# Performance work log

Measured on AMD Instinct MI355X. Metric: run time of the kernel, lower is better.

Reference implementation:

```python
import jax, jax.numpy as jnp
import numpy as np

GROUP_SIZE = 128
LORA_SCALING = 32.0 / 16.0  # lora_alpha / r


def _unpack_rows(q):
    # q: int32 [n, m] -> uint4 values [n*8, m], 8 nibbles per int32 along axis 0
    shifts = (jnp.arange(8, dtype=jnp.int32) * 4)
    vals = (q[:, None, :] >> shifts[None, :, None]) & 0xF
    return vals.reshape(q.shape[0] * 8, q.shape[1])


def _unpack_cols(q):
    # q: int32 [g, m] -> uint4 values [g, m*8], 8 nibbles per int32 along axis 1
    shifts = (jnp.arange(8, dtype=jnp.int32) * 4)
    vals = (q[:, :, None] >> shifts[None, None, :]) & 0xF
    return vals.reshape(q.shape[0], q.shape[1] * 8)


def setup_inputs() -> dict:
    key = jax.random.key(0)
    ks = jax.random.split(key, 6)
    in_f, out_f, tokens, r = 4096, 11008, 64, 16
    g = in_f // GROUP_SIZE  # 32 groups
    x = jax.random.normal(ks[0], (tokens, in_f), dtype=jnp.float32)
    qweight = jax.random.randint(ks[1], (in_f // 8, out_f), jnp.iinfo(jnp.int32).min, jnp.iinfo(jnp.int32).max, dtype=jnp.int32)
    qzeros = jax.random.randint(ks[2], (g, out_f // 8), jnp.iinfo(jnp.int32).min, jnp.iinfo(jnp.int32).max, dtype=jnp.int32)
    scales = jax.random.uniform(ks[3], (g, out_f), dtype=jnp.float32) * 0.01 + 0.001
    lora_A = jax.random.normal(ks[4], (r, in_f), dtype=jnp.float32) * 0.02
    lora_B = jax.random.normal(ks[5], (out_f, r), dtype=jnp.float32) * 0.02
    return {"x": x, "qweight": qweight, "qzeros": qzeros, "scales": scales,
            "lora_A": lora_A, "lora_B": lora_B}


def reference(x, qweight, qzeros, scales, lora_A, lora_B):
    in_f = qweight.shape[0] * 8
    # --- GPTQ int4 dequant ---
    wq = _unpack_rows(qweight).astype(jnp.float32)          # [in, out]
    zeros = (_unpack_cols(qzeros) + 1).astype(jnp.float32)  # [groups, out] (GPTQ +1 offset)
    g_idx = jnp.arange(in_f) // GROUP_SIZE                  # [in]
    W = scales[g_idx] * (wq - zeros[g_idx])                 # [in, out]
    # base quantized matmul
    result = x @ W                                          # [tokens, out]
    # --- LoRA adapter (single active adapter, dropout=0, tmp_weight=1) ---
    lora_out = (x @ lora_A.T) @ lora_B.T                    # [tokens, out]
    return result + lora_out * LORA_SCALING
```

## Files before the change

kernel.cpp:

```cpp
#include <hip/hip_runtime.h>
#include <stdint.h>

#define TOKENS 64
#define IN_F   4096
#define OUT_F  11008
#define RANK   16
#define GS     128
#define NG     32
#define ZCOLS  (OUT_F / 8)
#define LORA_SCALE 2.0f
#define GPK 8

using short8  = __attribute__((ext_vector_type(8))) short;
using float4v = __attribute__((ext_vector_type(4))) float;

static __device__ inline uint16_t f2bf(float f, float* back) {
    uint32_t u = __float_as_uint(f);
    uint32_t r = (u + 0x7FFFu + ((u >> 16) & 1u)) >> 16;
    *back = __uint_as_float(r << 16);
    return (uint16_t)r;
}

__global__ __launch_bounds__(256) void prep_kernel(
        const float* __restrict__ x,
        const float* __restrict__ loraA,
        uint4* __restrict__ xf4,
        float* __restrict__ xsumT,
        float* __restrict__ midT) {
    __shared__ float redg[256];
    __shared__ float redm[4][16];
    const int t    = blockIdx.x;
    const int tid  = threadIdx.x;
    const int lane = tid & 63;
    const int wv   = tid >> 6;

    float4 xv[4];
    const float4* xp = (const float4*)(x + (size_t)t * IN_F + tid * 16);
    #pragma unroll
    for (int i = 0; i < 4; ++i) xv[i] = xp[i];

    union { uint16_t u[16]; uint4 q[2]; } ob;
    float s = 0.f;
    #pragma unroll
    for (int i = 0; i < 4; ++i) {
        float b;
        ob.u[i * 4 + 0] = f2bf(xv[i].x, &b); s += b;
        ob.u[i * 4 + 1] = f2bf(xv[i].y, &b); s += b;
        ob.u[i * 4 + 2] = f2bf(xv[i].z, &b); s += b;
        ob.u[i * 4 + 3] = f2bf(xv[i].w, &b); s += b;
    }
    {
        const int mm = t >> 4, nn = t & 15;
        const int kchunk = tid >> 1;
        #pragma unroll
        for (int i = 0; i < 2; ++i) {
            const int qd = (tid * 2 + i) & 3;
            xf4[(size_t)((mm * 128 + kchunk) * 64 + qd * 16 + nn)] = ob.q[i];
        }
    }
    redg[tid] = s;

    float pj[16];
    #pragma unroll
    for (int j = 0; j < 16; ++j) {
        const float4* ap = (const float4*)(loraA + (size_t)j * IN_F + tid * 16);
        float ps = 0.f;
        #pragma unroll
        for (int i = 0; i < 4; ++i) {
            float4 a = ap[i];
            ps += a.x * xv[i].x + a.y * xv[i].y + a.z * xv[i].z + a.w * xv[i].w;
        }
        pj[j] = ps;
    }
    #pragma unroll
    for (int j = 0; j < 16; ++j) {
        #pragma unroll
        for (int off = 32; off; off >>= 1) pj[j] += __shfl_down(pj[j], off);
    }
    if (lane == 0) {
        #pragma unroll
        for (int j = 0; j < 16; ++j) redm[wv][j] = pj[j];
    }
    __syncthreads();
    if (tid < NG) {
        float g = 0.f;
        #pragma unroll
        for (int i = 0; i < 8; ++i) g += redg[tid * 8 + i];
        xsumT[tid * TOKENS + t] = g;
    }
    if (tid < 16)
        midT[tid * TOKENS + t] = redm[0][tid] + redm[1][tid] + redm[2][tid] + redm[3][tid];
}

#define PROW 34
#define PIDX(mhv, ksv, tlv) (((mhv) * 4 + (ksv)) * (32 * PROW) + (tlv) * PROW)

#define LOADB(sb, g) do {                                                       \
    _Pragma("unroll")                                                           \
    for (int ks = 0; ks < 4; ++ks)                                              \
        _Pragma("unroll")                                                       \
        for (int nh = 0; nh < 2; ++nh)                                          \
            B[sb][ks * 2 + nh] =                                                \
                qwc[(size_t)((g) * 16 + ks * 4 + quad) * OUT_F + nh * 16];      \
} while (0)

#define LOADA(sa, g) do {                                                       \
    _Pragma("unroll")                                                           \
    for (int mt = 0; mt < 2; ++mt)                                              \
        _Pragma("unroll")                                                       \
        for (int ks = 0; ks < 4; ++ks)                                          \
            A[sa][mt * 4 + ks] =                                                \
                xf4[(size_t)((((mh * 2 + mt) * 128 + (g) * 4 + ks) * 64)) + lane];\
    _Pragma("unroll")                                                           \
    for (int mt = 0; mt < 2; ++mt)                                              \
        XS[sa][mt] = *(const float4*)(xsumT + (g) * 64 +                        \
                                      (mh * 2 + mt) * 16 + quad * 4);           \
    _Pragma("unroll")                                                           \
    for (int nh = 0; nh < 2; ++nh) {                                            \
        S[sa][nh] = scales[(size_t)(g) * OUT_F + col0 + nh * 16 + n];           \
        Z[sa][nh] = qz[(size_t)(g) * ZCOLS + ((col0 + nh * 16 + n) >> 3)];      \
    }                                                                           \
} while (0)

#define COMPUTEG(sa, sb) do {                                                   \
    float4v accg[2][2];                                                         \
    _Pragma("unroll")                                                           \
    for (int mt = 0; mt < 2; ++mt)                                              \
        _Pragma("unroll")                                                       \
        for (int nh = 0; nh < 2; ++nh)                                          \
            accg[mt][nh] = (float4v){0.f, 0.f, 0.f, 0.f};                       \
    _Pragma("unroll")                                                           \
    for (int ks = 0; ks < 4; ++ks) {                                            \
        union { uint4 u; short8 s; } af0, af1;                                  \
        af0.u = A[sa][ks];                                                      \
        af1.u = A[sa][4 + ks];                                                  \
        _Pragma("unroll")                                                       \
        for (int nh = 0; nh < 2; ++nh) {                                        \
            uint32_t q  = B[sb][ks * 2 + nh];                                   \
            uint32_t lo = q & 0x0F0F0F0Fu;                                      \
            uint32_t hi = (q >> 4) & 0x0F0F0F0Fu;                               \
            union { uint32_t u32[4]; short8 s8; } bf;                           \
            _Pragma("unroll")                                                   \
            for (int i = 0; i < 4; ++i)                                         \
                bf.u32[i] = __builtin_amdgcn_perm(hi, lo,                       \
                                0x0C040C00u + i * 0x00010001u) | 0x43004300u;   \
            accg[0][nh] = __builtin_amdgcn_mfma_f32_16x16x32_bf16(af0.s, bf.s8, \
                                                            accg[0][nh], 0, 0, 0);\
            accg[1][nh] = __builtin_amdgcn_mfma_f32_16x16x32_bf16(af1.s, bf.s8, \
                                                            accg[1][nh], 0, 0, 0);\
        }                                                                       \
    }                                                                           \
    _Pragma("unroll")                                                           \
    for (int nh = 0; nh < 2; ++nh) {                                            \
        const float zoff = (float)(((Z[sa][nh] >>                               \
                        (((col0 + nh * 16 + n) & 7) * 4)) & 0xFu) + 129u);      \
        const float scl = S[sa][nh];                                            \
        _Pragma("unroll")                                                       \
        for (int mt = 0; mt < 2; ++mt) {                                        \
            const float xr[4] = {XS[sa][mt].x, XS[sa][mt].y,                    \
                                 XS[sa][mt].z, XS[sa][mt].w};                   \
            _Pragma("unroll")                                                   \
            for (int r = 0; r < 4; ++r)                                         \
                acc[mt][nh][r] = fmaf(scl, fmaf(-zoff, xr[r],                   \
                                      accg[mt][nh][r]), acc[mt][nh][r]);        \
        }                                                                       \
    }                                                                           \
} while (0)

__global__ __launch_bounds__(512, 3) void main_kernel(
        const uint32_t* __restrict__ qw,
        const uint32_t* __restrict__ qz,
        const float* __restrict__ scales,
        const uint4* __restrict__ xf4,
        const float* __restrict__ xsumT,
        const float* __restrict__ midT,
        const float* __restrict__ loraB,
        float* __restrict__ out) {
    __shared__ float part[2 * 4 * 32 * PROW];

    const int tid  = threadIdx.x;
    const int wv   = tid >> 6;
    const int lane = tid & 63;
    const int n    = lane & 15;
    const int quad = lane >> 4;
    const int mh   = wv >> 2;
    const int kseg = wv & 3;
    const int col0 = blockIdx.x * 32;
    const int g0   = kseg * GPK;

    const uint32_t* qwc = qw + col0 + n;

    float4v acc[2][2];
    #pragma unroll
    for (int mt = 0; mt < 2; ++mt)
        #pragma unroll
        for (int nh = 0; nh < 2; ++nh)
            acc[mt][nh] = (float4v){0.f, 0.f, 0.f, 0.f};

    uint4    A[2][8];
    uint32_t B[3][8];
    float4   XS[2][2];
    float    S[2][2];
    uint32_t Z[2][2];

    LOADB(0, g0); LOADB(1, g0 + 1); LOADB(2, g0 + 2);
    LOADA(0, g0); LOADA(1, g0 + 1);
    #pragma unroll
    for (int gi = 0; gi < GPK; ++gi) {
        const int sb = gi % 3, sa = gi & 1;
        COMPUTEG(sa, sb);
        if (gi + 3 < GPK) LOADB(sb, g0 + gi + 3);
        if (gi + 2 < GPK) LOADA(sa, g0 + gi + 2);
    }

    {
        float* pb = part + PIDX(mh, kseg, 0);
        #pragma unroll
        for (int mt = 0; mt < 2; ++mt)
            #pragma unroll
            for (int nh = 0; nh < 2; ++nh)
                #pragma unroll
                for (int r = 0; r < 4; ++r)
                    pb[(mt * 16 + quad * 4 + r) * PROW + nh * 16 + n] =
                        acc[mt][nh][r];
    }
    __syncthreads();

    {
        const int emh = tid >> 8;
        const int rem = tid & 255;
        const int tl  = rem >> 3;
        const int c4  = (rem & 7) * 4;
        const int t   = emh * 32 + tl;

        float4 sum = *(const float4*)&part[PIDX(emh, 0, tl) + c4];
        #pragma unroll
        for (int ks = 1; ks < 4; ++ks) {
            const float4 p = *(const float4*)&part[PIDX(emh, ks, tl) + c4];
            sum.x += p.x; sum.y += p.y; sum.z += p.z; sum.w += p.w;
        }

        float m[16];
        #pragma unroll
        for (int j = 0; j < 16; ++j) m[j] = midT[j * TOKENS + t];
        float ls[4];
        #pragma unroll
        for (int c = 0; c < 4; ++c) {
            const float4* b4 = (const float4*)(loraB + (size_t)(col0 + c4 + c) * RANK);
            float a = 0.f;
            #pragma unroll
            for (int i = 0; i < 4; ++i) {
                float4 b = b4[i];
                a += b.x * m[i * 4 + 0] + b.y * m[i * 4 + 1]
                   + b.z * m[i * 4 + 2] + b.w * m[i * 4 + 3];
            }
            ls[c] = a;
        }

        float4 o;
        o.x = sum.x + LORA_SCALE * ls[0];
        o.y = sum.y + LORA_SCALE * ls[1];
        o.z = sum.z + LORA_SCALE * ls[2];
        o.w = sum.w + LORA_SCALE * ls[3];
        *(float4*)(out + (size_t)t * OUT_F + col0 + c4) = o;
    }
}

extern "C" void kernel_launch(void* const* d_in, const int* in_sizes, int n_in,
                              void* d_out, int out_size, void* d_ws, size_t ws_size,
                              hipStream_t stream) {
    const float*    x      = (const float*)d_in[0];
    const uint32_t* qw     = (const uint32_t*)d_in[1];
    const uint32_t* qz     = (const uint32_t*)d_in[2];
    const float*    scales = (const float*)d_in[3];
    const float*    loraA  = (const float*)d_in[4];
    const float*    loraB  = (const float*)d_in[5];
    float* out = (float*)d_out;

    uint4* xf4   = (uint4*)d_ws;
    float* xsumT = (float*)((char*)d_ws + (size_t)TOKENS * IN_F * 2);
    float* midT  = xsumT + NG * TOKENS;

    prep_kernel<<<TOKENS, 256, 0, stream>>>(x, loraA, xf4, xsumT, midT);
    main_kernel<<<OUT_F / 32, 512, 0, stream>>>(qw, qz, scales, xf4, xsumT,
                                                midT, loraB, out);
}
```

Baseline: 118.8 us.

## Stage qweight tile through LDS with coalesced 16-byte loads and finer-grain pipelining

Each block now loads its whole 32-column qweight tile up front with coalesced uint4 loads into a 64KB shared buffer. It then feeds the MFMA loop from LDS instead of strided 4-byte global reads. Scales and zeros are preloaded into registers, and the A/B register pipeline is restructured per k-step. The launch-bounds occupancy hint rises from 3 to 4. The 64KB LDS per block may limit occupancy, and the up-front load serializes with compute because there is no overlap across blocks within a CU.

```diff
diff --git a/kernel.cpp b/kernel.cpp
--- a/kernel.cpp
+++ b/kernel.cpp
@@ -9,7 +9,7 @@
 #define NG     32
 #define ZCOLS  (OUT_F / 8)
 #define LORA_SCALE 2.0f
-#define GPK 8
+#define PROW 36
 
 using short8  = __attribute__((ext_vector_type(8))) short;
 using float4v = __attribute__((ext_vector_type(4))) float;
@@ -92,82 +92,7 @@
         midT[tid * TOKENS + t] = redm[0][tid] + redm[1][tid] + redm[2][tid] + redm[3][tid];
 }
 
-#define PROW 34
-#define PIDX(mhv, ksv, tlv) (((mhv) * 4 + (ksv)) * (32 * PROW) + (tlv) * PROW)
-
-#define LOADB(sb, g) do {                                                       \
-    _Pragma("unroll")                                                           \
-    for (int ks = 0; ks < 4; ++ks)                                              \
-        _Pragma("unroll")                                                       \
-        for (int nh = 0; nh < 2; ++nh)                                          \
-            B[sb][ks * 2 + nh] =                                                \
-                qwc[(size_t)((g) * 16 + ks * 4 + quad) * OUT_F + nh * 16];      \
-} while (0)
-
-#define LOADA(sa, g) do {                                                       \
-    _Pragma("unroll")                                                           \
-    for (int mt = 0; mt < 2; ++mt)                                              \
-        _Pragma("unroll")                                                       \
-        for (int ks = 0; ks < 4; ++ks)                                          \
-            A[sa][mt * 4 + ks] =                                                \
-                xf4[(size_t)((((mh * 2 + mt) * 128 + (g) * 4 + ks) * 64)) + lane];\
-    _Pragma("unroll")                                                           \
-    for (int mt = 0; mt < 2; ++mt)                                              \
-        XS[sa][mt] = *(const float4*)(xsumT + (g) * 64 +                        \
-                                      (mh * 2 + mt) * 16 + quad * 4);           \
-    _Pragma("unroll")                                                           \
-    for (int nh = 0; nh < 2; ++nh) {                                            \
-        S[sa][nh] = scales[(size_t)(g) * OUT_F + col0 + nh * 16 + n];           \
-        Z[sa][nh] = qz[(size_t)(g) * ZCOLS + ((col0 + nh * 16 + n) >> 3)];      \
-    }                                                                           \
-} while (0)
-
-#define COMPUTEG(sa, sb) do {                                                   \
-    float4v accg[2][2];                                                         \
-    _Pragma("unroll")                                                           \
-    for (int mt = 0; mt < 2; ++mt)                                              \
-        _Pragma("unroll")                                                       \
-        for (int nh = 0; nh < 2; ++nh)                                          \
-            accg[mt][nh] = (float4v){0.f, 0.f, 0.f, 0.f};                       \
-    _Pragma("unroll")                                                           \
-    for (int ks = 0; ks < 4; ++ks) {                                            \
-        union { uint4 u; short8 s; } af0, af1;                                  \
-        af0.u = A[sa][ks];                                                      \
-        af1.u = A[sa][4 + ks];                                                  \
-        _Pragma("unroll")                                                       \
-        for (int nh = 0; nh < 2; ++nh) {                                        \
-            uint32_t q  = B[sb][ks * 2 + nh];                                   \
-            uint32_t lo = q & 0x0F0F0F0Fu;                                      \
-            uint32_t hi = (q >> 4) & 0x0F0F0F0Fu;                               \
-            union { uint32_t u32[4]; short8 s8; } bf;                           \
-            _Pragma("unroll")                                                   \
-            for (int i = 0; i < 4; ++i)                                         \
-                bf.u32[i] = __builtin_amdgcn_perm(hi, lo,                       \
-                                0x0C040C00u + i * 0x00010001u) | 0x43004300u;   \
-            accg[0][nh] = __builtin_amdgcn_mfma_f32_16x16x32_bf16(af0.s, bf.s8, \
-                                                            accg[0][nh], 0, 0, 0);\
-            accg[1][nh] = __builtin_amdgcn_mfma_f32_16x16x32_bf16(af1.s, bf.s8, \
-                                                            accg[1][nh], 0, 0, 0);\
-        }                                                                       \
-    }                                                                           \
-    _Pragma("unroll")                                                           \
-    for (int nh = 0; nh < 2; ++nh) {                                            \
-        const float zoff = (float)(((Z[sa][nh] >>                               \
-                        (((col0 + nh * 16 + n) & 7) * 4)) & 0xFu) + 129u);      \
-        const float scl = S[sa][nh];                                            \
-        _Pragma("unroll")                                                       \
-        for (int mt = 0; mt < 2; ++mt) {                                        \
-            const float xr[4] = {XS[sa][mt].x, XS[sa][mt].y,                    \
-                                 XS[sa][mt].z, XS[sa][mt].w};                   \
-            _Pragma("unroll")                                                   \
-            for (int r = 0; r < 4; ++r)                                         \
-                acc[mt][nh][r] = fmaf(scl, fmaf(-zoff, xr[r],                   \
-                                      accg[mt][nh][r]), acc[mt][nh][r]);        \
-        }                                                                       \
-    }                                                                           \
-} while (0)
-
-__global__ __launch_bounds__(512, 3) void main_kernel(
+__global__ __launch_bounds__(512, 4) void main_kernel(
         const uint32_t* __restrict__ qw,
         const uint32_t* __restrict__ qz,
         const float* __restrict__ scales,
@@ -176,19 +101,41 @@
         const float* __restrict__ midT,
         const float* __restrict__ loraB,
         float* __restrict__ out) {
-    __shared__ float part[2 * 4 * 32 * PROW];
+    __shared__ uint32_t smem[16384];
 
     const int tid  = threadIdx.x;
-    const int wv   = tid >> 6;
+    const int w    = tid >> 6;
     const int lane = tid & 63;
     const int n    = lane & 15;
     const int quad = lane >> 4;
-    const int mh   = wv >> 2;
-    const int kseg = wv & 3;
+    const int mh   = w >> 2;
+    const int kseg = w & 3;
     const int col0 = blockIdx.x * 32;
-    const int g0   = kseg * GPK;
-
-    const uint32_t* qwc = qw + col0 + n;
+    const int g0   = kseg * 8;
+
+    uint4 stg[8];
+    #pragma unroll
+    for (int i = 0; i < 8; ++i) {
+        const int t   = w * 8 + i;
+        const int row = (t >> 1) * 16 + (t & 1) * 8 + (lane >> 3);
+        stg[i] = *(const uint4*)(qw + (size_t)row * OUT_F + col0 + (lane & 7) * 4);
+    }
+    float    Scr[8][2];
+    uint32_t Zqr[8][2];
+    #pragma unroll
+    for (int gp = 0; gp < 8; ++gp)
+        #pragma unroll
+        for (int nh = 0; nh < 2; ++nh) {
+            Scr[gp][nh] = scales[(size_t)(g0 + gp) * OUT_F + col0 + nh * 16 + n];
+            Zqr[gp][nh] = qz[(size_t)(g0 + gp) * ZCOLS + ((col0 + nh * 16 + n) >> 3)];
+        }
+    #pragma unroll
+    for (int i = 0; i < 8; ++i)
+        *(uint4*)&smem[(w * 8 + i) * 256 + lane * 4] = stg[i];
+    __syncthreads();
+
+    const int abase = mh * 16384 + kseg * 2048 + lane;
+    const int bbase = kseg * 4096 + quad * 32 + n;
 
     float4v acc[2][2];
     #pragma unroll
@@ -196,36 +143,93 @@
         #pragma unroll
         for (int nh = 0; nh < 2; ++nh)
             acc[mt][nh] = (float4v){0.f, 0.f, 0.f, 0.f};
-
-    uint4    A[2][8];
-    uint32_t B[3][8];
-    float4   XS[2][2];
-    float    S[2][2];
-    uint32_t Z[2][2];
-
-    LOADB(0, g0); LOADB(1, g0 + 1); LOADB(2, g0 + 2);
-    LOADA(0, g0); LOADA(1, g0 + 1);
-    #pragma unroll
-    for (int gi = 0; gi < GPK; ++gi) {
-        const int sb = gi % 3, sa = gi & 1;
-        COMPUTEG(sa, sb);
-        if (gi + 3 < GPK) LOADB(sb, g0 + gi + 3);
-        if (gi + 2 < GPK) LOADA(sa, g0 + gi + 2);
-    }
-
+    float4v accg[2][2];
+    uint4    AR[3][2];
+    uint32_t Bw[2][2];
+    float4   XS[2];
+
+    #pragma unroll
+    for (int s = 0; s < 3; ++s) {
+        AR[s][0] = xf4[abase + s * 64];
+        AR[s][1] = xf4[abase + 8192 + s * 64];
+    }
+    #pragma unroll
+    for (int b = 0; b < 2; ++b) {
+        Bw[b][0] = smem[bbase + b * 128];
+        Bw[b][1] = smem[bbase + b * 128 + 16];
+    }
+
+    #pragma unroll
+    for (int kk = 0; kk < 32; ++kk) {
+        const int s  = kk % 3;
+        const int b  = kk & 1;
+        const int ks = kk & 3;
+        const int gp = kk >> 2;
+        if (ks == 0) {
+            #pragma unroll
+            for (int mt = 0; mt < 2; ++mt) {
+                XS[mt] = *(const float4*)(xsumT + (g0 + gp) * 64 +
+                                          (mh * 2 + mt) * 16 + quad * 4);
+                accg[mt][0] = (float4v){0.f, 0.f, 0.f, 0.f};
+                accg[mt][1] = (float4v){0.f, 0.f, 0.f, 0.f};
+            }
+        }
+        union { uint4 u; short8 s; } a0, a1;
+        a0.u = AR[s][0];
+        a1.u = AR[s][1];
+        #pragma unroll
+        for (int nh = 0; nh < 2; ++nh) {
+            const uint32_t q  = Bw[b][nh];
+            const uint32_t lo = q & 0x0F0F0F0Fu;
+            const uint32_t hi = (q >> 4) & 0x0F0F0F0Fu;
+            union { uint32_t u32[4]; short8 s8; } bf;
+            #pragma unroll
+            for (int i = 0; i < 4; ++i)
+                bf.u32[i] = __builtin_amdgcn_perm(hi, lo, 0x0C040C00u + i * 0x00010001u)
+                            | 0x43004300u;
+            accg[0][nh] = __builtin_amdgcn_mfma_f32_16x16x32_bf16(a0.s, bf.s8,
+                                                                  accg[0][nh], 0, 0, 0);
+            accg[1][nh] = __builtin_amdgcn_mfma_f32_16x16x32_bf16(a1.s, bf.s8,
+                                                                  accg[1][nh], 0, 0, 0);
+        }
+        if (kk + 3 < 32) {
+            AR[s][0] = xf4[abase + (kk + 3) * 64];
+            AR[s][1] = xf4[abase + 8192 + (kk + 3) * 64];
+        }
+        if (kk + 2 < 32) {
+            Bw[b][0] = smem[bbase + (kk + 2) * 128];
+            Bw[b][1] = smem[bbase + (kk + 2) * 128 + 16];
+        }
+        if (ks == 3) {
+            #pragma unroll
+            for (int nh = 0; nh < 2; ++nh) {
+                const float zoff = (float)(((Zqr[gp][nh] >> ((n & 7) * 4)) & 0xFu) + 129u);
+                const float scl  = Scr[gp][nh];
+                #pragma unroll
+                for (int mt = 0; mt < 2; ++mt) {
+                    const float xr[4] = {XS[mt].x, XS[mt].y, XS[mt].z, XS[mt].w};
+                    #pragma unroll
+                    for (int r = 0; r < 4; ++r)
+                        acc[mt][nh][r] = fmaf(scl, fmaf(-zoff, xr[r], accg[mt][nh][r]),
+                                              acc[mt][nh][r]);
+                }
+            }
+        }
+    }
+
+    __syncthreads();
+    float* part = (float*)smem;
     {
-        float* pb = part + PIDX(mh, kseg, 0);
+        float* pb = part + (mh * 4 + kseg) * (32 * PROW);
         #pragma unroll
         for (int mt = 0; mt < 2; ++mt)
             #pragma unroll
             for (int nh = 0; nh < 2; ++nh)
                 #pragma unroll
                 for (int r = 0; r < 4; ++r)
-                    pb[(mt * 16 + quad * 4 + r) * PROW + nh * 16 + n] =
-                        acc[mt][nh][r];
-    }
-    __syncthreads();
-
+                    pb[(mt * 16 + quad * 4 + r) * PROW + nh * 16 + n] = acc[mt][nh][r];
+    }
+    __syncthreads();
     {
         const int emh = tid >> 8;
         const int rem = tid & 255;
@@ -233,10 +237,11 @@
         const int c4  = (rem & 7) * 4;
         const int t   = emh * 32 + tl;
 
-        float4 sum = *(const float4*)&part[PIDX(emh, 0, tl) + c4];
+        float4 sum = *(const float4*)&part[(emh * 4) * (32 * PROW) + tl * PROW + c4];
         #pragma unroll
         for (int ks = 1; ks < 4; ++ks) {
-            const float4 p = *(const float4*)&part[PIDX(emh, ks, tl) + c4];
+            const float4 p = *(const float4*)&part[(emh * 4 + ks) * (32 * PROW)
+                                                   + tl * PROW + c4];
             sum.x += p.x; sum.y += p.y; sum.z += p.z; sum.w += p.w;
         }
 
@@ -250,9 +255,9 @@
             float a = 0.f;
             #pragma unroll
             for (int i = 0; i < 4; ++i) {
-                float4 b = b4[i];
-                a += b.x * m[i * 4 + 0] + b.y * m[i * 4 + 1]
-                   + b.z * m[i * 4 + 2] + b.w * m[i * 4 + 3];
+                float4 bv = b4[i];
+                a += bv.x * m[i * 4 + 0] + bv.y * m[i * 4 + 1]
+                   + bv.z * m[i * 4 + 2] + bv.w * m[i * 4 + 3];
             }
             ls[c] = a;
         }
```

Result: slower. 142.7 us (+20.1%).
